# Kernel tuning notes

Measured on AMD Instinct MI355X. Metric: run time of the kernel, lower is better.

Reference implementation:

```python
import jax, jax.numpy as jnp
import numpy as np

EMBED_DIM = 256
NUM_HEADS = 4
HEAD_DIM = EMBED_DIM // NUM_HEADS
SCALE = HEAD_DIM ** (-0.5)


def setup_inputs() -> dict:
    key = jax.random.key(0)
    kx, kq, kp, kb = jax.random.split(key, 4)
    B, N, C = 4, 4096, EMBED_DIM
    x = jax.random.normal(kx, (B, N, C), dtype=jnp.float32)
    # qkv: Linear(C, 3C, bias=False); torch stores weight as [out, in]
    w_qkv = jax.random.normal(kq, (3 * C, C), dtype=jnp.float32) * (C ** -0.5)
    w_proj = jax.random.normal(kp, (C, C), dtype=jnp.float32) * (C ** -0.5)
    b_proj = jax.random.normal(kb, (C,), dtype=jnp.float32) * 0.01
    return {"x": x, "w_qkv": w_qkv, "w_proj": w_proj, "b_proj": b_proj}


def reference(x, w_qkv, w_proj, b_proj):
    B, N, C = x.shape
    H, D = NUM_HEADS, HEAD_DIM
    # qkv projection: [B,N,3C] -> [3,B,H,N,D]
    qkv = (x @ w_qkv.T).reshape(B, N, 3, H, D).transpose(2, 0, 3, 1, 4)
    q, k, v = qkv[0], qkv[1], qkv[2]
    # materialized [B,H,N,N] scores (faithful to the original)
    attn = jnp.einsum("bhnd,bhmd->bhnm", q, k) * SCALE
    attn_probs = jax.nn.softmax(attn, axis=-1)
    out = jnp.einsum("bhnm,bhmd->bhnd", attn_probs, v)
    out = out.transpose(0, 2, 1, 3).reshape(B, N, C)
    return out @ w_proj.T + b_proj
```

## Files before the change

kernel.cpp:

```cpp
#include <hip/hip_runtime.h>
#include <hip/hip_bf16.h>

typedef __hip_bfloat16 bf16;
typedef _Float16 f16;
typedef __attribute__((ext_vector_type(8))) short bf16x8;
typedef __attribute__((ext_vector_type(8))) _Float16 f16x8;
typedef __attribute__((ext_vector_type(2))) _Float16 f16x2;
typedef __attribute__((ext_vector_type(4))) float f32x4;
typedef __attribute__((ext_vector_type(4))) unsigned int u32x4;
typedef __attribute__((ext_vector_type(2))) unsigned int u32x2;

#define B_ 4
#define N_ 4096
#define C_ 256
#define H_ 4
#define D_ 64
#define KLN 0.18033688011112042f

#if __has_builtin(__builtin_amdgcn_exp2f)
#define EXP2(x) __builtin_amdgcn_exp2f(x)
#else
#define EXP2(x) exp2f(x)
#endif
#if __has_builtin(__builtin_amdgcn_rcpf)
#define RCP(x) __builtin_amdgcn_rcpf(x)
#else
#define RCP(x) (1.0f / (x))
#endif

__device__ inline void load_lds16(const void* g, void* l) {
#if __has_builtin(__builtin_amdgcn_global_load_lds)
    __builtin_amdgcn_global_load_lds(
        (const __attribute__((address_space(1))) unsigned int*)g,
        (__attribute__((address_space(3))) unsigned int*)l, 16, 0, 0);
#else
    int ln = __lane_id();
    ((u32x4*)l)[ln] = *((const u32x4*)g);
#endif
}

__device__ inline unsigned int pk2(float a, float b) {
    unsigned int ua = __builtin_bit_cast(unsigned int, a) + 0x8000u;
    unsigned int ub = __builtin_bit_cast(unsigned int, b) + 0x8000u;
    return (ua >> 16) | (ub & 0xffff0000u);
}
__device__ inline unsigned int pkh2(float a, float b) {
#if __has_builtin(__builtin_amdgcn_cvt_pkrtz)
    return __builtin_bit_cast(unsigned int, __builtin_amdgcn_cvt_pkrtz(a, b));
#else
    f16x2 h = { (f16)a, (f16)b };
    return __builtin_bit_cast(unsigned int, h);
#endif
}

__global__ __launch_bounds__(256) void cast_bf16(const float* __restrict__ x,
                                                 const float* __restrict__ wq,
                                                 const float* __restrict__ wp,
                                                 bf16* __restrict__ xb,
                                                 bf16* __restrict__ wqb,
                                                 bf16* __restrict__ wpb)
{
    int bid = blockIdx.x;
    const float* s; bf16* d; int base;
    if (bid < 2048)      { s = x;  d = xb;  base = bid * 2048; }
    else if (bid < 2144) { s = wq; d = wqb; base = (bid - 2048) * 2048; }
    else                 { s = wp; d = wpb; base = (bid - 2144) * 2048; }
    int i = base + threadIdx.x * 8;
    f32x4 a = *reinterpret_cast<const f32x4*>(s + i);
    f32x4 b = *reinterpret_cast<const f32x4*>(s + i + 4);
    u32x4 o;
    o.x = pk2(a[0], a[1]); o.y = pk2(a[2], a[3]);
    o.z = pk2(b[0], b[1]); o.w = pk2(b[2], b[3]);
    *reinterpret_cast<u32x4*>(d + i) = o;
}

__global__ __launch_bounds__(256, 2) void qkv_fast(const bf16* __restrict__ x,
                                                   const bf16* __restrict__ w,
                                                   bf16* __restrict__ qw,
                                                   bf16* __restrict__ kw,
                                                   f16* __restrict__ vtw)
{
    __shared__ short w_s[64][264];
    const int tid  = threadIdx.x;
    const int lane = tid & 63;
    const int wav  = tid >> 6;
    const int quad = lane >> 4;
    const int l16  = lane & 15;
    const int bid = (blockIdx.x & 7) * 192 + (blockIdx.x >> 3);
    const int mt = bid / 12, nb = bid % 12;
    const int m0 = mt * 128, n0 = nb * 64;

    {
        const int row = tid >> 2, cb = (tid & 3) * 64;
        const bf16* src = w + (size_t)(n0 + row) * C_ + cb;
#pragma unroll
        for (int i = 0; i < 8; ++i)
            *reinterpret_cast<bf16x8*>(&w_s[row][cb + i * 8]) =
                *reinterpret_cast<const bf16x8*>(src + i * 8);
    }
    __syncthreads();

#pragma unroll
    for (int half = 0; half < 2; ++half) {
        const int mh = m0 + half * 64;
        f32x4 acc[4] = {{0,0,0,0},{0,0,0,0},{0,0,0,0},{0,0,0,0}};
        const bf16* xrow = x + (size_t)(mh + wav * 16 + l16) * C_ + quad * 8;
        if (nb < 8) {
#pragma unroll
            for (int k0 = 0; k0 < C_; k0 += 32) {
                bf16x8 a = *reinterpret_cast<const bf16x8*>(xrow + k0);
#pragma unroll
                for (int nt = 0; nt < 4; ++nt) {
                    bf16x8 b = *reinterpret_cast<const bf16x8*>(&w_s[nt * 16 + l16][k0 + quad * 8]);
                    acc[nt] = __builtin_amdgcn_mfma_f32_16x16x32_bf16(b, a, acc[nt], 0, 0, 0);
                }
            }
        } else {
#pragma unroll
            for (int k0 = 0; k0 < C_; k0 += 32) {
                bf16x8 a = *reinterpret_cast<const bf16x8*>(xrow + k0);
#pragma unroll
                for (int nt = 0; nt < 4; ++nt) {
                    bf16x8 b = *reinterpret_cast<const bf16x8*>(&w_s[nt * 16 + l16][k0 + quad * 8]);
                    acc[nt] = __builtin_amdgcn_mfma_f32_16x16x32_bf16(a, b, acc[nt], 0, 0, 0);
                }
            }
        }

        const int bb = mh >> 12;
        const int nbase = (mh + wav * 16) & (N_ - 1);
        if (nb < 4) {
            bf16* dst = qw + (((size_t)bb * H_ + nb) * N_ + nbase + l16) * D_;
#pragma unroll
            for (int nt = 0; nt < 4; ++nt) {
                u32x2 wv = { pk2(acc[nt][0] * KLN, acc[nt][1] * KLN),
                             pk2(acc[nt][2] * KLN, acc[nt][3] * KLN) };
                *reinterpret_cast<u32x2*>(dst + nt * 16 + quad * 4) = wv;
            }
        } else if (nb < 8) {
            bf16* dst = kw + (((size_t)bb * H_ + (nb - 4)) * N_ + nbase + l16) * D_;
#pragma unroll
            for (int nt = 0; nt < 4; ++nt) {
                u32x2 wv = { pk2(acc[nt][0], acc[nt][1]),
                             pk2(acc[nt][2], acc[nt][3]) };
                *reinterpret_cast<u32x2*>(dst + nt * 16 + quad * 4) = wv;
            }
        } else {
            const int h = nb - 8;
#pragma unroll
            for (int nt = 0; nt < 4; ++nt) {
                int d = nt * 16 + l16;
                u32x2 wv;
                wv.x = pkh2(acc[nt][0], acc[nt][1]);
                wv.y = pkh2(acc[nt][2], acc[nt][3]);
                *reinterpret_cast<u32x2*>(
                    vtw + (((size_t)bb * H_ + h) * D_ + d) * N_ + nbase + quad * 4) = wv;
            }
        }
    }
}

__global__ __launch_bounds__(512, 4) void attn(const bf16* __restrict__ q,
                                               const bf16* __restrict__ k,
                                               const f16* __restrict__ vt,
                                               bf16* __restrict__ o)
{
    __shared__ __align__(16) char smem[65536];
    short* k_s = reinterpret_cast<short*>(smem);
    f16*   v_s = reinterpret_cast<f16*>(smem + 32768);

    const int tid  = threadIdx.x;
    const int lane = tid & 63;
    const int wav  = tid >> 6;
    const int quad = lane >> 4;
    const int l16  = lane & 15;
    const int l8   = lane & 7;
    const int sub  = wav & 3;
    const int jh   = wav >> 2;

    const int wg = (blockIdx.x & 7) * 64 + (blockIdx.x >> 3);
    const int bh = wg >> 5;
    const int qt = wg & 31;
    const int bb = bh >> 2, h = bh & 3;

    const bf16* qp = q  + (size_t)bh * N_ * D_;
    const bf16* kp = k  + (size_t)bh * N_ * D_;
    const f16*  vp = vt + (size_t)bh * D_ * N_;

    const int qbase = qt * 128 + sub * 32;
    bf16x8 qb[2][2];
#pragma unroll
    for (int qg = 0; qg < 2; ++qg)
#pragma unroll
        for (int ks = 0; ks < 2; ++ks)
            qb[qg][ks] = *reinterpret_cast<const bf16x8*>(
                qp + (size_t)(qbase + qg * 16 + l16) * D_ + ks * 32 + quad * 8);

    const int ri = lane >> 3;
    const int ci = lane & 7;
    const int gc = ci ^ ri;
    int koff[2], voff[2], lds_r[2];
#pragma unroll
    for (int g = 0; g < 2; ++g) {
        const int rb  = sub * 16 + g * 8;
        const int rho = rb + ri;
        const int pr  = (rho & 32) | ((rho & 12) << 1) | ((rho & 16) >> 2) | (rho & 3);
        koff[g]  = pr * D_ + gc * 8;
        voff[g]  = rho * N_ + gc * 8;
        lds_r[g] = rb * 64;
    }

    f32x4 oacc[2][4];
    f32x4 lacc[2];
#pragma unroll
    for (int qg = 0; qg < 2; ++qg) {
        lacc[qg] = (f32x4){0, 0, 0, 0};
#pragma unroll
        for (int dt = 0; dt < 4; ++dt) oacc[qg][dt] = (f32x4){0, 0, 0, 0};
    }
    const f16x8 onesA = {1.f16, 1.f16, 1.f16, 1.f16, 1.f16, 1.f16, 1.f16, 1.f16};

    auto stage = [&](int buf, int t) {
        const int j0 = jh * 2048 + t * 64;
        short* kd = k_s + (size_t)(buf * 2 + jh) * 4096;
        f16*   vd = v_s + (size_t)(buf * 2 + jh) * 4096;
#pragma unroll
        for (int g = 0; g < 2; ++g) {
            load_lds16(kp + (size_t)j0 * D_ + koff[g], kd + lds_r[g]);
            load_lds16(vp + j0 + voff[g],              vd + lds_r[g]);
        }
    };

    stage(0, 0);
    __syncthreads();

    for (int t = 0; t < 32; ++t) {
        const int cur = t & 1;
        if (t < 31) stage(cur ^ 1, t + 1);

        const short* kt  = k_s + (size_t)(cur * 2 + jh) * 4096;
        const f16*   vtl = v_s + (size_t)(cur * 2 + jh) * 4096;

        bf16x8 ka[4][2];
#pragma unroll
        for (int nt = 0; nt < 4; ++nt) {
            const int rb = (nt * 16 + l16) * 64;
            ka[nt][0] = *reinterpret_cast<const bf16x8*>(kt + rb + ((quad    ) ^ l8) * 8);
            ka[nt][1] = *reinterpret_cast<const bf16x8*>(kt + rb + ((4 + quad) ^ l8) * 8);
        }

        f32x4 s[4];
        f16x8 pb0[2], pb1[2];

#pragma unroll
        for (int nt = 0; nt < 4; ++nt) {
            s[nt] = __builtin_amdgcn_mfma_f32_16x16x32_bf16(
                ka[nt][0], qb[0][0], (f32x4){0.f, 0.f, 0.f, 0.f}, 0, 0, 0);
            s[nt] = __builtin_amdgcn_mfma_f32_16x16x32_bf16(
                ka[nt][1], qb[0][1], s[nt], 0, 0, 0);
        }
#pragma unroll
        for (int ks = 0; ks < 2; ++ks) {
            const f32x4 sa = s[2 * ks], sb = s[2 * ks + 1];
            u32x4 pw;
            pw.x = pkh2(EXP2(sa[0]), EXP2(sa[1]));
            pw.y = pkh2(EXP2(sa[2]), EXP2(sa[3]));
            pw.z = pkh2(EXP2(sb[0]), EXP2(sb[1]));
            pw.w = pkh2(EXP2(sb[2]), EXP2(sb[3]));
            pb0[ks] = __builtin_bit_cast(f16x8, pw);
            lacc[0] = __builtin_amdgcn_mfma_f32_16x16x32_f16(onesA, pb0[ks], lacc[0], 0, 0, 0);
        }
#pragma unroll
        for (int nt = 0; nt < 4; ++nt) {
            s[nt] = __builtin_amdgcn_mfma_f32_16x16x32_bf16(
                ka[nt][0], qb[1][0], (f32x4){0.f, 0.f, 0.f, 0.f}, 0, 0, 0);
            s[nt] = __builtin_amdgcn_mfma_f32_16x16x32_bf16(
                ka[nt][1], qb[1][1], s[nt], 0, 0, 0);
        }
#pragma unroll
        for (int ks = 0; ks < 2; ++ks)
#pragma unroll
            for (int dt = 0; dt < 4; ++dt) {
                f16x8 va = *reinterpret_cast<const f16x8*>(
                    vtl + (dt * 16 + l16) * 64 + (((ks << 2) + quad) ^ l8) * 8);
                oacc[0][dt] = __builtin_amdgcn_mfma_f32_16x16x32_f16(va, pb0[ks], oacc[0][dt], 0, 0, 0);
            }
#pragma unroll
        for (int ks = 0; ks < 2; ++ks) {
            const f32x4 sa = s[2 * ks], sb = s[2 * ks + 1];
            u32x4 pw;
            pw.x = pkh2(EXP2(sa[0]), EXP2(sa[1]));
            pw.y = pkh2(EXP2(sa[2]), EXP2(sa[3]));
            pw.z = pkh2(EXP2(sb[0]), EXP2(sb[1]));
            pw.w = pkh2(EXP2(sb[2]), EXP2(sb[3]));
            pb1[ks] = __builtin_bit_cast(f16x8, pw);
            lacc[1] = __builtin_amdgcn_mfma_f32_16x16x32_f16(onesA, pb1[ks], lacc[1], 0, 0, 0);
        }
#pragma unroll
        for (int ks = 0; ks < 2; ++ks)
#pragma unroll
            for (int dt = 0; dt < 4; ++dt) {
                f16x8 va = *reinterpret_cast<const f16x8*>(
                    vtl + (dt * 16 + l16) * 64 + (((ks << 2) + quad) ^ l8) * 8);
                oacc[1][dt] = __builtin_amdgcn_mfma_f32_16x16x32_f16(va, pb1[ks], oacc[1][dt], 0, 0, 0);
            }

        __syncthreads();
    }

    __syncthreads();
    float* mrg = reinterpret_cast<float*>(smem);
    const int slot = (sub * 64 + lane) * 35;
    if (jh == 1) {
#pragma unroll
        for (int qg = 0; qg < 2; ++qg) {
#pragma unroll
            for (int dt = 0; dt < 4; ++dt)
#pragma unroll
                for (int e = 0; e < 4; ++e)
                    mrg[slot + qg * 17 + dt * 4 + e] = oacc[qg][dt][e];
            mrg[slot + qg * 17 + 16] = lacc[qg][0];
        }
    }
    __syncthreads();
    if (jh == 0) {
#pragma unroll
        for (int qg = 0; qg < 2; ++qg) {
            const float rl = RCP(lacc[qg][0] + mrg[slot + qg * 17 + 16]);
            const size_t obase = ((size_t)bb * N_ + qbase + qg * 16 + l16) * C_ + h * D_;
#pragma unroll
            for (int dt = 0; dt < 4; ++dt) {
                float v0 = (oacc[qg][dt][0] + mrg[slot + qg * 17 + dt * 4 + 0]) * rl;
                float v1 = (oacc[qg][dt][1] + mrg[slot + qg * 17 + dt * 4 + 1]) * rl;
                float v2 = (oacc[qg][dt][2] + mrg[slot + qg * 17 + dt * 4 + 2]) * rl;
                float v3 = (oacc[qg][dt][3] + mrg[slot + qg * 17 + dt * 4 + 3]) * rl;
                u32x2 wv = { pk2(v0, v1), pk2(v2, v3) };
                *reinterpret_cast<u32x2*>(o + obase + dt * 16 + quad * 4) = wv;
            }
        }
    }
}

__global__ __launch_bounds__(256, 2) void out_proj_fast(const bf16* __restrict__ ov,
                                                        const bf16* __restrict__ w,
                                                        const float* __restrict__ bias,
                                                        float* __restrict__ out)
{
    __shared__ short w_s[64][264];
    const int tid  = threadIdx.x;
    const int lane = tid & 63;
    const int wav  = tid >> 6;
    const int quad = lane >> 4;
    const int l16  = lane & 15;
    const int bid = (blockIdx.x & 7) * 64 + (blockIdx.x >> 3);
    const int m0 = (bid >> 2) * 128;
    const int n0 = (bid & 3) * 64;

    {
        const int row = tid >> 2, cb = (tid & 3) * 64;
        const bf16* src = w + (size_t)(n0 + row) * C_ + cb;
#pragma unroll
        for (int i = 0; i < 8; ++i)
            *reinterpret_cast<bf16x8*>(&w_s[row][cb + i * 8]) =
                *reinterpret_cast<const bf16x8*>(src + i * 8);
    }
    __syncthreads();

#pragma unroll
    for (int half = 0; half < 2; ++half) {
        const int mh = m0 + half * 64;
        f32x4 acc[4] = {{0,0,0,0},{0,0,0,0},{0,0,0,0},{0,0,0,0}};
        const bf16* orow = ov + (size_t)(mh + wav * 16 + l16) * C_ + quad * 8;
#pragma unroll
        for (int k0 = 0; k0 < C_; k0 += 32) {
            bf16x8 a = *reinterpret_cast<const bf16x8*>(orow + k0);
#pragma unroll
            for (int nt = 0; nt < 4; ++nt) {
                bf16x8 b = *reinterpret_cast<const bf16x8*>(&w_s[nt * 16 + l16][k0 + quad * 8]);
                acc[nt] = __builtin_amdgcn_mfma_f32_16x16x32_bf16(b, a, acc[nt], 0, 0, 0);
            }
        }
        const int m = mh + wav * 16 + l16;
#pragma unroll
        for (int nt = 0; nt < 4; ++nt) {
            const int oc0 = n0 + nt * 16 + quad * 4;
            f32x4 bv = *reinterpret_cast<const f32x4*>(bias + oc0);
            f32x4 ovv = acc[nt] + bv;
            *reinterpret_cast<f32x4*>(out + (size_t)m * C_ + oc0) = ovv;
        }
    }
}

extern "C" void kernel_launch(void* const* d_in, const int* in_sizes, int n_in,
                              void* d_out, int out_size, void* d_ws, size_t ws_size,
                              hipStream_t stream) {
    const float* x      = (const float*)d_in[0];
    const float* w_qkv  = (const float*)d_in[1];
    const float* w_proj = (const float*)d_in[2];
    const float* b_proj = (const float*)d_in[3];
    float* out = (float*)d_out;

    const size_t qkv_elems = (size_t)B_ * H_ * N_ * D_;
    bf16* q_ws  = (bf16*)d_ws;
    bf16* k_ws  = q_ws  + qkv_elems;
    f16*  vt_ws = (f16*)(k_ws + qkv_elems);
    bf16* o_ws  = (bf16*)(vt_ws + qkv_elems);
    bf16* x_bf  = o_ws  + qkv_elems;
    bf16* wq_bf = x_bf  + (size_t)B_ * N_ * C_;
    bf16* wp_bf = wq_bf + (size_t)3 * C_ * C_;

    cast_bf16    <<<2176, 256, 0, stream>>>(x, w_qkv, w_proj, x_bf, wq_bf, wp_bf);
    qkv_fast     <<<1536, 256, 0, stream>>>(x_bf, wq_bf, q_ws, k_ws, vt_ws);
    attn         <<< 512, 512, 0, stream>>>(q_ws, k_ws, vt_ws, o_ws);
    out_proj_fast<<< 512, 256, 0, stream>>>(o_ws, wp_bf, b_proj, out);
}
```

Before: 173.0 us.

## Unroll double-buffered KV loop by two with precomputed pointers and reordered PV

```diff
diff --git a/kernel.cpp b/kernel.cpp
--- a/kernel.cpp
+++ b/kernel.cpp
@@ -199,16 +199,38 @@
     const int ri = lane >> 3;
     const int ci = lane & 7;
     const int gc = ci ^ ri;
-    int koff[2], voff[2], lds_r[2];
-#pragma unroll
-    for (int g = 0; g < 2; ++g) {
-        const int rb  = sub * 16 + g * 8;
-        const int rho = rb + ri;
-        const int pr  = (rho & 32) | ((rho & 12) << 1) | ((rho & 16) >> 2) | (rho & 3);
-        koff[g]  = pr * D_ + gc * 8;
-        voff[g]  = rho * N_ + gc * 8;
-        lds_r[g] = rb * 64;
-    }
+    const int rb0 = sub * 16;
+    const int rb1 = sub * 16 + 8;
+    const int rho0 = rb0 + ri, rho1 = rb1 + ri;
+    const int pr0 = (rho0 & 32) | ((rho0 & 12) << 1) | ((rho0 & 16) >> 2) | (rho0 & 3);
+    const int pr1 = (rho1 & 32) | ((rho1 & 12) << 1) | ((rho1 & 16) >> 2) | (rho1 & 3);
+
+    const int j00 = jh * 2048;
+
+    const bf16* ksrc0 = kp + (size_t)(j00 + 64) * D_ + pr0 * D_ + gc * 8;
+    const bf16* ksrc1 = kp + (size_t)(j00 + 64) * D_ + pr1 * D_ + gc * 8;
+    const f16*  vsrc0 = vp + (size_t)rho0 * N_ + j00 + 64 + gc * 8;
+    const f16*  vsrc1 = vp + (size_t)rho1 * N_ + j00 + 64 + gc * 8;
+
+    short* kdst0g0 = k_s + (0 * 2 + jh) * 4096 + rb0 * 64;
+    short* kdst0g1 = k_s + (0 * 2 + jh) * 4096 + rb1 * 64;
+    short* kdst1g0 = k_s + (1 * 2 + jh) * 4096 + rb0 * 64;
+    short* kdst1g1 = k_s + (1 * 2 + jh) * 4096 + rb1 * 64;
+    f16* vdst0g0 = v_s + (0 * 2 + jh) * 4096 + rb0 * 64;
+    f16* vdst0g1 = v_s + (0 * 2 + jh) * 4096 + rb1 * 64;
+    f16* vdst1g0 = v_s + (1 * 2 + jh) * 4096 + rb0 * 64;
+    f16* vdst1g1 = v_s + (1 * 2 + jh) * 4096 + rb1 * 64;
+
+    const int fragA = l16 * 64 + ((quad    ) ^ l8) * 8;
+    const int fragB = l16 * 64 + ((4 + quad) ^ l8) * 8;
+    const short* kb0A = k_s + (0 * 2 + jh) * 4096 + fragA;
+    const short* kb0B = k_s + (0 * 2 + jh) * 4096 + fragB;
+    const short* kb1A = k_s + (1 * 2 + jh) * 4096 + fragA;
+    const short* kb1B = k_s + (1 * 2 + jh) * 4096 + fragB;
+    const f16* vb0A = v_s + (0 * 2 + jh) * 4096 + fragA;
+    const f16* vb0B = v_s + (0 * 2 + jh) * 4096 + fragB;
+    const f16* vb1A = v_s + (1 * 2 + jh) * 4096 + fragA;
+    const f16* vb1B = v_s + (1 * 2 + jh) * 4096 + fragB;
 
     f32x4 oacc[2][4];
     f32x4 lacc[2];
@@ -220,92 +242,72 @@
     }
     const f16x8 onesA = {1.f16, 1.f16, 1.f16, 1.f16, 1.f16, 1.f16, 1.f16, 1.f16};
 
-    auto stage = [&](int buf, int t) {
-        const int j0 = jh * 2048 + t * 64;
-        short* kd = k_s + (size_t)(buf * 2 + jh) * 4096;
-        f16*   vd = v_s + (size_t)(buf * 2 + jh) * 4096;
-#pragma unroll
-        for (int g = 0; g < 2; ++g) {
-            load_lds16(kp + (size_t)j0 * D_ + koff[g], kd + lds_r[g]);
-            load_lds16(vp + j0 + voff[g],              vd + lds_r[g]);
-        }
+    load_lds16(ksrc0 - 64 * D_, kdst0g0);
+    load_lds16(ksrc1 - 64 * D_, kdst0g1);
+    load_lds16(vsrc0 - 64,      vdst0g0);
+    load_lds16(vsrc1 - 64,      vdst0g1);
+    __syncthreads();
+
+    auto tile_body = [&](const short* kbA, const short* kbB,
+                         const f16* vbA, const f16* vbB,
+                         short* kdg0, short* kdg1, f16* vdg0, f16* vdg1,
+                         bool do_stage) {
+        if (do_stage) {
+            load_lds16(ksrc0, kdg0);
+            load_lds16(ksrc1, kdg1);
+            load_lds16(vsrc0, vdg0);
+            load_lds16(vsrc1, vdg1);
+            ksrc0 += 64 * D_; ksrc1 += 64 * D_;
+            vsrc0 += 64;      vsrc1 += 64;
+        }
+
+        bf16x8 ka[4][2];
+#pragma unroll
+        for (int nt = 0; nt < 4; ++nt) {
+            ka[nt][0] = *reinterpret_cast<const bf16x8*>(kbA + nt * 1024);
+            ka[nt][1] = *reinterpret_cast<const bf16x8*>(kbB + nt * 1024);
+        }
+
+        f16x8 pb[2][2];
+#pragma unroll
+        for (int qg = 0; qg < 2; ++qg) {
+            f32x4 s[4];
+#pragma unroll
+            for (int nt = 0; nt < 4; ++nt) {
+                s[nt] = __builtin_amdgcn_mfma_f32_16x16x32_bf16(
+                    ka[nt][0], qb[qg][0], (f32x4){0.f, 0.f, 0.f, 0.f}, 0, 0, 0);
+                s[nt] = __builtin_amdgcn_mfma_f32_16x16x32_bf16(
+                    ka[nt][1], qb[qg][1], s[nt], 0, 0, 0);
+            }
+#pragma unroll
+            for (int ks = 0; ks < 2; ++ks) {
+                const f32x4 sa = s[2 * ks], sb = s[2 * ks + 1];
+                u32x4 pw;
+                pw.x = pkh2(EXP2(sa[0]), EXP2(sa[1]));
+                pw.y = pkh2(EXP2(sa[2]), EXP2(sa[3]));
+                pw.z = pkh2(EXP2(sb[0]), EXP2(sb[1]));
+                pw.w = pkh2(EXP2(sb[2]), EXP2(sb[3]));
+                pb[qg][ks] = __builtin_bit_cast(f16x8, pw);
+                lacc[qg] = __builtin_amdgcn_mfma_f32_16x16x32_f16(onesA, pb[qg][ks], lacc[qg], 0, 0, 0);
+            }
+        }
+
+#pragma unroll
+        for (int dt = 0; dt < 4; ++dt) {
+            f16x8 va0 = *reinterpret_cast<const f16x8*>(vbA + dt * 1024);
+            oacc[0][dt] = __builtin_amdgcn_mfma_f32_16x16x32_f16(va0, pb[0][0], oacc[0][dt], 0, 0, 0);
+            oacc[1][dt] = __builtin_amdgcn_mfma_f32_16x16x32_f16(va0, pb[1][0], oacc[1][dt], 0, 0, 0);
+            f16x8 va1 = *reinterpret_cast<const f16x8*>(vbB + dt * 1024);
+            oacc[0][dt] = __builtin_amdgcn_mfma_f32_16x16x32_f16(va1, pb[0][1], oacc[0][dt], 0, 0, 0);
+            oacc[1][dt] = __builtin_amdgcn_mfma_f32_16x16x32_f16(va1, pb[1][1], oacc[1][dt], 0, 0, 0);
+        }
+
+        __syncthreads();
     };
 
-    stage(0, 0);
-    __syncthreads();
-
-    for (int t = 0; t < 32; ++t) {
-        const int cur = t & 1;
-        if (t < 31) stage(cur ^ 1, t + 1);
-
-        const short* kt  = k_s + (size_t)(cur * 2 + jh) * 4096;
-        const f16*   vtl = v_s + (size_t)(cur * 2 + jh) * 4096;
-
-        bf16x8 ka[4][2];
-#pragma unroll
-        for (int nt = 0; nt < 4; ++nt) {
-            const int rb = (nt * 16 + l16) * 64;
-            ka[nt][0] = *reinterpret_cast<const bf16x8*>(kt + rb + ((quad    ) ^ l8) * 8);
-            ka[nt][1] = *reinterpret_cast<const bf16x8*>(kt + rb + ((4 + quad) ^ l8) * 8);
-        }
-
-        f32x4 s[4];
-        f16x8 pb0[2], pb1[2];
-
-#pragma unroll
-        for (int nt = 0; nt < 4; ++nt) {
-            s[nt] = __builtin_amdgcn_mfma_f32_16x16x32_bf16(
-                ka[nt][0], qb[0][0], (f32x4){0.f, 0.f, 0.f, 0.f}, 0, 0, 0);
-            s[nt] = __builtin_amdgcn_mfma_f32_16x16x32_bf16(
-                ka[nt][1], qb[0][1], s[nt], 0, 0, 0);
-        }
-#pragma unroll
-        for (int ks = 0; ks < 2; ++ks) {
-            const f32x4 sa = s[2 * ks], sb = s[2 * ks + 1];
-            u32x4 pw;
-            pw.x = pkh2(EXP2(sa[0]), EXP2(sa[1]));
-            pw.y = pkh2(EXP2(sa[2]), EXP2(sa[3]));
-            pw.z = pkh2(EXP2(sb[0]), EXP2(sb[1]));
-            pw.w = pkh2(EXP2(sb[2]), EXP2(sb[3]));
-            pb0[ks] = __builtin_bit_cast(f16x8, pw);
-            lacc[0] = __builtin_amdgcn_mfma_f32_16x16x32_f16(onesA, pb0[ks], lacc[0], 0, 0, 0);
-        }
-#pragma unroll
-        for (int nt = 0; nt < 4; ++nt) {
-            s[nt] = __builtin_amdgcn_mfma_f32_16x16x32_bf16(
-                ka[nt][0], qb[1][0], (f32x4){0.f, 0.f, 0.f, 0.f}, 0, 0, 0);
-            s[nt] = __builtin_amdgcn_mfma_f32_16x16x32_bf16(
-                ka[nt][1], qb[1][1], s[nt], 0, 0, 0);
-        }
-#pragma unroll
-        for (int ks = 0; ks < 2; ++ks)
-#pragma unroll
-            for (int dt = 0; dt < 4; ++dt) {
-                f16x8 va = *reinterpret_cast<const f16x8*>(
-                    vtl + (dt * 16 + l16) * 64 + (((ks << 2) + quad) ^ l8) * 8);
-                oacc[0][dt] = __builtin_amdgcn_mfma_f32_16x16x32_f16(va, pb0[ks], oacc[0][dt], 0, 0, 0);
-            }
-#pragma unroll
-        for (int ks = 0; ks < 2; ++ks) {
-            const f32x4 sa = s[2 * ks], sb = s[2 * ks + 1];
-            u32x4 pw;
-            pw.x = pkh2(EXP2(sa[0]), EXP2(sa[1]));
-            pw.y = pkh2(EXP2(sa[2]), EXP2(sa[3]));
-            pw.z = pkh2(EXP2(sb[0]), EXP2(sb[1]));
-            pw.w = pkh2(EXP2(sb[2]), EXP2(sb[3]));
-            pb1[ks] = __builtin_bit_cast(f16x8, pw);
-            lacc[1] = __builtin_amdgcn_mfma_f32_16x16x32_f16(onesA, pb1[ks], lacc[1], 0, 0, 0);
-        }
-#pragma unroll
-        for (int ks = 0; ks < 2; ++ks)
-#pragma unroll
-            for (int dt = 0; dt < 4; ++dt) {
-                f16x8 va = *reinterpret_cast<const f16x8*>(
-                    vtl + (dt * 16 + l16) * 64 + (((ks << 2) + quad) ^ l8) * 8);
-                oacc[1][dt] = __builtin_amdgcn_mfma_f32_16x16x32_f16(va, pb1[ks], oacc[1][dt], 0, 0, 0);
-            }
-
-        __syncthreads();
+    for (int tt = 0; tt < 16; ++tt) {
+        tile_body(kb0A, kb0B, vb0A, vb0B, kdst1g0, kdst1g1, vdst1g0, vdst1g1, true);
+        tile_body(kb1A, kb1B, vb1A, vb1B, kdst0g0, kdst0g1, vdst0g0, vdst0g1, tt < 15);
     }
 
     __syncthreads();
```

Measured after the change: 174.6 us. No clear change (+1.0%).

## Software-pipeline attention loop: overlap QK of next tile with PV of previous

Applied to the files above, without the earlier changes.

```diff
diff --git a/kernel.cpp b/kernel.cpp
--- a/kernel.cpp
+++ b/kernel.cpp
@@ -165,7 +165,7 @@
                                                const f16* __restrict__ vt,
                                                bf16* __restrict__ o)
 {
-    __shared__ __align__(16) char smem[65536];
+    __shared__ __align__(16) char smem[81920];
     short* k_s = reinterpret_cast<short*>(smem);
     f16*   v_s = reinterpret_cast<f16*>(smem + 32768);
 
@@ -220,10 +220,10 @@
     }
     const f16x8 onesA = {1.f16, 1.f16, 1.f16, 1.f16, 1.f16, 1.f16, 1.f16, 1.f16};
 
-    auto stage = [&](int buf, int t) {
+    auto stageKV = [&](int kbuf, int vslot, int t) {
         const int j0 = jh * 2048 + t * 64;
-        short* kd = k_s + (size_t)(buf * 2 + jh) * 4096;
-        f16*   vd = v_s + (size_t)(buf * 2 + jh) * 4096;
+        short* kd = k_s + (size_t)(kbuf * 2 + jh) * 4096;
+        f16*   vd = v_s + (size_t)(vslot * 2 + jh) * 4096;
 #pragma unroll
         for (int g = 0; g < 2; ++g) {
             load_lds16(kp + (size_t)j0 * D_ + koff[g], kd + lds_r[g]);
@@ -231,16 +231,11 @@
         }
     };
 
-    stage(0, 0);
-    __syncthreads();
-
-    for (int t = 0; t < 32; ++t) {
-        const int cur = t & 1;
-        if (t < 31) stage(cur ^ 1, t + 1);
-
-        const short* kt  = k_s + (size_t)(cur * 2 + jh) * 4096;
-        const f16*   vtl = v_s + (size_t)(cur * 2 + jh) * 4096;
-
+    f32x4 s[2][4];
+    f16x8 pbE[2][2], pbO[2][2];
+
+    auto qk = [&](int kbuf) {
+        const short* kt = k_s + (size_t)(kbuf * 2 + jh) * 4096;
         bf16x8 ka[4][2];
 #pragma unroll
         for (int nt = 0; nt < 4; ++nt) {
@@ -248,69 +243,88 @@
             ka[nt][0] = *reinterpret_cast<const bf16x8*>(kt + rb + ((quad    ) ^ l8) * 8);
             ka[nt][1] = *reinterpret_cast<const bf16x8*>(kt + rb + ((4 + quad) ^ l8) * 8);
         }
-
-        f32x4 s[4];
-        f16x8 pb0[2], pb1[2];
-
-#pragma unroll
-        for (int nt = 0; nt < 4; ++nt) {
-            s[nt] = __builtin_amdgcn_mfma_f32_16x16x32_bf16(
-                ka[nt][0], qb[0][0], (f32x4){0.f, 0.f, 0.f, 0.f}, 0, 0, 0);
-            s[nt] = __builtin_amdgcn_mfma_f32_16x16x32_bf16(
-                ka[nt][1], qb[0][1], s[nt], 0, 0, 0);
-        }
-#pragma unroll
-        for (int ks = 0; ks < 2; ++ks) {
-            const f32x4 sa = s[2 * ks], sb = s[2 * ks + 1];
-            u32x4 pw;
-            pw.x = pkh2(EXP2(sa[0]), EXP2(sa[1]));
-            pw.y = pkh2(EXP2(sa[2]), EXP2(sa[3]));
-            pw.z = pkh2(EXP2(sb[0]), EXP2(sb[1]));
-            pw.w = pkh2(EXP2(sb[2]), EXP2(sb[3]));
-            pb0[ks] = __builtin_bit_cast(f16x8, pw);
-            lacc[0] = __builtin_amdgcn_mfma_f32_16x16x32_f16(onesA, pb0[ks], lacc[0], 0, 0, 0);
-        }
-#pragma unroll
-        for (int nt = 0; nt < 4; ++nt) {
-            s[nt] = __builtin_amdgcn_mfma_f32_16x16x32_bf16(
-                ka[nt][0], qb[1][0], (f32x4){0.f, 0.f, 0.f, 0.f}, 0, 0, 0);
-            s[nt] = __builtin_amdgcn_mfma_f32_16x16x32_bf16(
-                ka[nt][1], qb[1][1], s[nt], 0, 0, 0);
-        }
+#pragma unroll
+        for (int qg = 0; qg < 2; ++qg)
+#pragma unroll
+            for (int nt = 0; nt < 4; ++nt) {
+                s[qg][nt] = __builtin_amdgcn_mfma_f32_16x16x32_bf16(
+                    ka[nt][0], qb[qg][0], (f32x4){0.f, 0.f, 0.f, 0.f}, 0, 0, 0);
+                s[qg][nt] = __builtin_amdgcn_mfma_f32_16x16x32_bf16(
+                    ka[nt][1], qb[qg][1], s[qg][nt], 0, 0, 0);
+            }
+    };
+
+    auto pv = [&](int vslot, f16x8 (*pb)[2]) {
+        const f16* vtl = v_s + (size_t)(vslot * 2 + jh) * 4096;
+#pragma unroll
+        for (int qg = 0; qg < 2; ++qg)
+#pragma unroll
+            for (int ks = 0; ks < 2; ++ks)
+                lacc[qg] = __builtin_amdgcn_mfma_f32_16x16x32_f16(onesA, pb[qg][ks], lacc[qg], 0, 0, 0);
 #pragma unroll
         for (int ks = 0; ks < 2; ++ks)
 #pragma unroll
             for (int dt = 0; dt < 4; ++dt) {
                 f16x8 va = *reinterpret_cast<const f16x8*>(
                     vtl + (dt * 16 + l16) * 64 + (((ks << 2) + quad) ^ l8) * 8);
-                oacc[0][dt] = __builtin_amdgcn_mfma_f32_16x16x32_f16(va, pb0[ks], oacc[0][dt], 0, 0, 0);
-            }
-#pragma unroll
-        for (int ks = 0; ks < 2; ++ks) {
-            const f32x4 sa = s[2 * ks], sb = s[2 * ks + 1];
-            u32x4 pw;
-            pw.x = pkh2(EXP2(sa[0]), EXP2(sa[1]));
-            pw.y = pkh2(EXP2(sa[2]), EXP2(sa[3]));
-            pw.z = pkh2(EXP2(sb[0]), EXP2(sb[1]));
-            pw.w = pkh2(EXP2(sb[2]), EXP2(sb[3]));
-            pb1[ks] = __builtin_bit_cast(f16x8, pw);
-            lacc[1] = __builtin_amdgcn_mfma_f32_16x16x32_f16(onesA, pb1[ks], lacc[1], 0, 0, 0);
-        }
-#pragma unroll
-        for (int ks = 0; ks < 2; ++ks)
-#pragma unroll
-            for (int dt = 0; dt < 4; ++dt) {
-                f16x8 va = *reinterpret_cast<const f16x8*>(
-                    vtl + (dt * 16 + l16) * 64 + (((ks << 2) + quad) ^ l8) * 8);
-                oacc[1][dt] = __builtin_amdgcn_mfma_f32_16x16x32_f16(va, pb1[ks], oacc[1][dt], 0, 0, 0);
-            }
-
-        __syncthreads();
-    }
+                oacc[0][dt] = __builtin_amdgcn_mfma_f32_16x16x32_f16(va, pb[0][ks], oacc[0][dt], 0, 0, 0);
+                oacc[1][dt] = __builtin_amdgcn_mfma_f32_16x16x32_f16(va, pb[1][ks], oacc[1][dt], 0, 0, 0);
+            }
+    };
+
+    auto expp = [&](f16x8 (*pb)[2]) {
+#pragma unroll
+        for (int qg = 0; qg < 2; ++qg)
+#pragma unroll
+            for (int ks = 0; ks < 2; ++ks) {
+                const f32x4 sa = s[qg][2 * ks], sb2 = s[qg][2 * ks + 1];
+                u32x4 pw;
+                pw.x = pkh2(EXP2(sa[0]), EXP2(sa[1]));
+                pw.y = pkh2(EXP2(sa[2]), EXP2(sa[3]));
+                pw.z = pkh2(EXP2(sb2[0]), EXP2(sb2[1]));
+                pw.w = pkh2(EXP2(sb2[2]), EXP2(sb2[3]));
+                pb[qg][ks] = __builtin_bit_cast(f16x8, pw);
+            }
+    };
+
+    stageKV(0, 0, 0);
+    __syncthreads();
+
+    stageKV(1, 1, 1);
+    qk(0); expp(pbE);
+    __syncthreads();
+
+    stageKV(0, 2, 2);
+    qk(1); pv(0, pbE); expp(pbO);
+    __syncthreads();
+
+#pragma unroll 1
+    for (int tb = 2; tb < 32; tb += 6) {
+        stageKV(1, 0, tb + 1);
+        qk(0); pv(1, pbO); expp(pbE);
+        __syncthreads();
+        stageKV(0, 1, tb + 2);
+        qk(1); pv(2, pbE); expp(pbO);
+        __syncthreads();
+        stageKV(1, 2, tb + 3);
+        qk(0); pv(0, pbO); expp(pbE);
+        __syncthreads();
+        stageKV(0, 0, tb + 4);
+        qk(1); pv(1, pbE); expp(pbO);
+        __syncthreads();
+        stageKV(1, 1, tb + 5);
+        qk(0); pv(2, pbO); expp(pbE);
+        __syncthreads();
+        if (tb + 6 < 32) stageKV(0, 2, tb + 6);
+        qk(1); pv(0, pbE); expp(pbO);
+        __syncthreads();
+    }
+    pv(1, pbO);
 
     __syncthreads();
     float* mrg = reinterpret_cast<float*>(smem);
     const int slot = (sub * 64 + lane) * 35;
+    float lr[2] = { lacc[0][0], lacc[1][0] };
     if (jh == 1) {
 #pragma unroll
         for (int qg = 0; qg < 2; ++qg) {
@@ -319,14 +333,14 @@
 #pragma unroll
                 for (int e = 0; e < 4; ++e)
                     mrg[slot + qg * 17 + dt * 4 + e] = oacc[qg][dt][e];
-            mrg[slot + qg * 17 + 16] = lacc[qg][0];
+            mrg[slot + qg * 17 + 16] = lr[qg];
         }
     }
     __syncthreads();
     if (jh == 0) {
 #pragma unroll
         for (int qg = 0; qg < 2; ++qg) {
-            const float rl = RCP(lacc[qg][0] + mrg[slot + qg * 17 + 16]);
+            const float rl = RCP(lr[qg] + mrg[slot + qg * 17 + 16]);
             const size_t obase = ((size_t)bb * N_ + qbase + qg * 16 + l16) * C_ + h * D_;
 #pragma unroll
             for (int dt = 0; dt < 4; ++dt) {
```

Result: slower. 262.0 us (+51.5%).
